# Performance work log

Hardware: AMD Instinct MI355X
Metric: run time of the kernel (lower is better)

The kernel has to match this reference:

```python
import jax, jax.numpy as jnp
import numpy as np

IOU_THRESHOLD = 0.5
CLASS_CONF_THRESHOLD = 0.01
MAX_OUTPUT = 100  # tf.image.non_max_suppression max_output_size


def _nms_indices(boxes, scores, max_out, iou_thr):
    """Fixed-size greedy NMS: returns (idxs[max_out], valid[max_out])."""
    x1, y1, x2, y2 = boxes[:, 0], boxes[:, 1], boxes[:, 2], boxes[:, 3]
    areas = (x2 - x1) * (y2 - y1)

    def body(sc, _):
        i = jnp.argmax(sc)
        valid = sc[i] > 0.0  # score_threshold = 0.0 in tf call
        xx1 = jnp.maximum(x1[i], x1)
        yy1 = jnp.maximum(y1[i], y1)
        xx2 = jnp.minimum(x2[i], x2)
        yy2 = jnp.minimum(y2[i], y2)
        inter = jnp.maximum(xx2 - xx1, 0.0) * jnp.maximum(yy2 - yy1, 0.0)
        union = areas[i] + areas - inter
        iou = jnp.where(union > 0.0, inter / union, 0.0)
        # suppress overlapping boxes (self included, iou=1) only if pick valid
        sc_new = jnp.where((iou > iou_thr) & valid, -1.0, sc)
        return sc_new, (i, valid)

    _, (idxs, valids) = jax.lax.scan(body, scores, None, length=max_out)
    return idxs, valids


def _decode(x, anchors):
    B, H, W, A, C = x.shape  # B == 1
    gw = jnp.float32(W)
    # grid offsets: (col, row) per cell, matching cell_x / transposed cell_y
    cx = jnp.broadcast_to(jnp.arange(W, dtype=jnp.float32).reshape(1, 1, W, 1, 1), (1, H, W, 1, 1))
    cy = jnp.broadcast_to(jnp.arange(H, dtype=jnp.float32).reshape(1, H, 1, 1, 1), (1, H, W, 1, 1))
    grid = jnp.concatenate([cx, cy], axis=-1)  # (1,H,W,1,2)

    xy = (jax.nn.sigmoid(x[..., 0:2]) + grid) / gw                      # (B,H,W,A,2)
    wh = jnp.exp(x[..., 2:4]) * anchors.reshape(1, 1, 1, A, 2) / gw     # (B,H,W,A,2)
    boxes = jnp.concatenate([xy - wh / 2.0, xy + wh / 2.0], axis=-1)    # (B,H,W,A,4)

    conf = jax.nn.sigmoid(x[..., 4:5])                                  # (B,H,W,A,1)
    cls_prob = jax.nn.softmax(x[..., 5:], axis=-1)                      # (B,H,W,A,C-5)
    class_confidence = conf * cls_prob
    masked = jnp.where(class_confidence > CLASS_CONF_THRESHOLD, class_confidence, 0.0)
    classes = jnp.argmax(masked, axis=-1).astype(jnp.int32)             # (B,H,W,A)
    confm = jnp.max(masked, axis=-1)                                    # (B,H,W,A)

    N = H * W * A
    return boxes.reshape(N, 4), confm.reshape(N), classes.reshape(N)


def reference(x, anchors):
    boxes, scores, classes = _decode(x, anchors)
    idxs, valids = _nms_indices(jax.lax.stop_gradient(boxes),
                                jax.lax.stop_gradient(scores),
                                MAX_OUTPUT, IOU_THRESHOLD)
    sel_conf = jnp.where(valids, scores[idxs], 0.0)
    sel_boxes = jnp.where(valids[:, None], boxes[idxs], 0.0)
    sel_classes = jnp.where(valids, classes[idxs], -1)
    return sel_conf, sel_boxes, sel_classes


def setup_inputs() -> dict:
    key = jax.random.key(0)
    k1, k2 = jax.random.split(key)
    x = jax.random.normal(k1, (1, 256, 256, 5, 85), dtype=jnp.float32)
    # anchor priors in grid units (positive widths/heights)
    anchors = jax.random.uniform(k2, (5, 2), dtype=jnp.float32) * 4.0 + 0.5
    return {"x": x, "anchors": anchors}
```

## Files before the change

kernel.cpp:

```cpp
#include <hip/hip_runtime.h>
#include <hip/hip_bf16.h>

#define NROW 327680
#define NCLS 80
#define K_TARGET 1024u
#define CAP 2048u
#define MAXN 2048
#define MAX_OUT 100
#define NBIN 864
#define BIN0 0x3C23
#define HIST_BLOCKS 80
#define ADJW 32
#define ADJC_ROWS 128

#define WS_SCORES 0
#define WS_PART   1310720
#define WS_CNT    1587200
#define WS_KEYS   1587264
#define WS_SORT   1603648
#define WS_CBOX   1620032
#define WS_ADJ    1652800

typedef float f4v __attribute__((ext_vector_type(4)));
typedef f4v f4u __attribute__((aligned(4)));
typedef unsigned long long ull;

__global__ __launch_bounds__(256, 5) void decode_score(
    const float* __restrict__ x, float* __restrict__ scores) {
  __shared__ float sc[24][256];
  const int t = threadIdx.x;
  const int r = blockIdx.x * 256 + t;
  const float* rp = x + (size_t)r * 85;

  float conf_l = rp[4];

  float cl[56];
  #pragma unroll
  for (int k = 0; k < 14; ++k) {
    f4v t4 = *(const f4u*)(rp + 5 + 4 * k);
    cl[4*k+0] = t4.x; cl[4*k+1] = t4.y; cl[4*k+2] = t4.z; cl[4*k+3] = t4.w;
  }
  #pragma unroll
  for (int k = 14; k < 20; ++k) {
    f4v t4 = *(const f4u*)(rp + 5 + 4 * k);
    sc[4*(k-14)+0][t] = t4.x; sc[4*(k-14)+1][t] = t4.y;
    sc[4*(k-14)+2][t] = t4.z; sc[4*(k-14)+3][t] = t4.w;
  }

  float m = cl[0];
  #pragma unroll
  for (int c = 1; c < 56; ++c) { float l = cl[c]; if (l > m) m = l; }
  #pragma unroll
  for (int c = 56; c < 80; ++c) { float l = sc[c-56][t]; if (l > m) m = l; }

  float s = 0.f;
  #pragma unroll
  for (int c = 0; c < 56; ++c) s += expf(cl[c] - m);
  #pragma unroll
  for (int c = 56; c < 80; ++c) s += expf(sc[c-56][t] - m);

  float conf = 1.f / (1.f + expf(-conf_l));
  float best = conf * (1.f / s);
  scores[r] = (best > 0.01f) ? best : 0.f;
}

__global__ __launch_bounds__(1024) void hist_kernel(
    const float* __restrict__ scores, unsigned* __restrict__ part) {
  __shared__ unsigned h[NBIN];
  const int t = threadIdx.x;
  if (t < NBIN) h[t] = 0;
  __syncthreads();

  float4 s4 = ((const float4*)scores)[blockIdx.x * 1024 + t];
  float sv[4] = {s4.x, s4.y, s4.z, s4.w};
  #pragma unroll
  for (int k = 0; k < 4; ++k) {
    float s = sv[k];
    if (s > 0.f) {
      int idx = (int)(__float_as_uint(s) >> 16) - BIN0;
      if (idx > NBIN - 1) idx = NBIN - 1;
      atomicAdd(&h[idx], 1u);
    }
  }
  __syncthreads();
  if (t < NBIN) part[blockIdx.x * NBIN + t] = h[t];
}

__global__ __launch_bounds__(1024) void thresh_kernel(
    const unsigned* __restrict__ part, unsigned* __restrict__ cnt) {
  __shared__ unsigned bufA[1024], bufB[1024];
  const int t = threadIdx.x;

  unsigned colsum = 0;
  if (t < NBIN) {
    unsigned a0 = 0, a1 = 0, a2 = 0, a3 = 0;
    #pragma unroll
    for (int b = 0; b < HIST_BLOCKS; b += 4) {
      a0 += part[(b + 0) * NBIN + t];
      a1 += part[(b + 1) * NBIN + t];
      a2 += part[(b + 2) * NBIN + t];
      a3 += part[(b + 3) * NBIN + t];
    }
    colsum = a0 + a1 + a2 + a3;
  }
  bufA[t] = colsum;
  __syncthreads();

  unsigned* src = bufA; unsigned* dst = bufB;
  for (int d = 1; d < 1024; d <<= 1) {
    unsigned val = src[t] + ((t + d < 1024) ? src[t + d] : 0u);
    dst[t] = val;
    __syncthreads();
    unsigned* tmp = src; src = dst; dst = tmp;
  }
  if (src[t] >= K_TARGET && (t == 1023 || src[t + 1] < K_TARGET)) {
    unsigned T = (unsigned)t;
    if (src[t] > CAP) T += 1;
    cnt[1] = T;
  }
  if (t == 0) {
    if (src[0] < K_TARGET) cnt[1] = 0;
    cnt[0] = 0;
  }
}

__global__ __launch_bounds__(256) void compact_kernel(
    const float* __restrict__ scores, unsigned* __restrict__ cnt,
    ull* __restrict__ keys) {
  __shared__ unsigned blocal, bbase;
  const int t = threadIdx.x;
  if (t == 0) blocal = 0;
  __syncthreads();

  const unsigned T = cnt[1];
  const int gi = blockIdx.x * 256 + t;
  float4 s4 = ((const float4*)scores)[gi];
  float sv[4] = {s4.x, s4.y, s4.z, s4.w};
  ull lk[4]; int nl = 0;
  #pragma unroll
  for (int k = 0; k < 4; ++k) {
    float s = sv[k];
    if (s <= 0.f) continue;
    unsigned bits = __float_as_uint(s);
    int idx = (int)(bits >> 16) - BIN0;
    if (idx > NBIN - 1) idx = NBIN - 1;
    if ((unsigned)idx < T) continue;
    unsigned r = (unsigned)(gi * 4 + k);
    lk[nl++] = ((ull)bits << 32) | (ull)(0xFFFFFFFFu - r);
  }
  unsigned lpos = nl ? atomicAdd(&blocal, (unsigned)nl) : 0u;
  __syncthreads();
  if (t == 0 && blocal) bbase = atomicAdd(&cnt[0], blocal);
  __syncthreads();
  if (nl) {
    unsigned base = bbase + lpos;
    for (int i = 0; i < nl; ++i)
      if (base + i < CAP) keys[base + i] = lk[i];
  }
}

__global__ __launch_bounds__(64) void rank_kernel(
    const float* __restrict__ x, const float* __restrict__ anchors,
    const unsigned* __restrict__ cnt, const ull* __restrict__ keys,
    ull* __restrict__ sorted, float4* __restrict__ cboxg) {
  __shared__ ull lk[MAXN];
  unsigned n = cnt[0]; if (n > CAP) n = CAP;
  const int t = threadIdx.x;
  for (unsigned i = t; i < n; i += 64) lk[i] = keys[i];
  __syncthreads();

  const unsigned i = blockIdx.x * 64 + t;
  if (i >= n) return;
  const ull ki = lk[i];
  unsigned rank = 0;
  #pragma unroll 4
  for (unsigned j = 0; j < n; ++j) rank += (lk[j] > ki) ? 1u : 0u;

  sorted[rank] = ki;

  unsigned r = 0xFFFFFFFFu - (unsigned)(ki & 0xFFFFFFFFull);
  const float* rp = x + (size_t)r * 85;
  float tx = rp[0], ty = rp[1], tw = rp[2], th = rp[3];
  const int a  = (int)(r % 5u);
  const int hw = (int)(r / 5u);
  const float wf = (float)(hw & 255);
  const float hf = (float)(hw >> 8);
  float sx = 1.f / (1.f + expf(-tx));
  float sy = 1.f / (1.f + expf(-ty));
  float xc = (sx + wf) / 256.f;
  float yc = (sy + hf) / 256.f;
  float bw = expf(tw) * anchors[2*a]     / 256.f;
  float bh = expf(th) * anchors[2*a + 1] / 256.f;
  float hwd = bw / 2.f, hhd = bh / 2.f;
  cboxg[rank] = make_float4(xc - hwd, yc - hhd, xc + hwd, yc + hhd);
}

__global__ __launch_bounds__(256) void adj_kernel(
    const unsigned* __restrict__ cnt, const float4* __restrict__ cboxg,
    ull* __restrict__ adj) {
  unsigned n = cnt[0]; if (n > CAP) n = CAP;
  const unsigned i = blockIdx.x;
  if (i >= n) return;
  const float4 bi = cboxg[i];
  const float areai = (bi.z - bi.x) * (bi.w - bi.y);
  const int t = threadIdx.x, wid = t >> 6, lane = t & 63;

  #pragma unroll
  for (int pass = 0; pass < 8; ++pass) {
    unsigned j = (unsigned)(pass * 256 + t);
    bool sup = false;
    if (j < n) {
      float4 bj = cboxg[j];
      float xx1 = fmaxf(bi.x, bj.x), yy1 = fmaxf(bi.y, bj.y);
      float xx2 = fminf(bi.z, bj.z), yy2 = fminf(bi.w, bj.w);
      float inter = fmaxf(xx2 - xx1, 0.f) * fmaxf(yy2 - yy1, 0.f);
      float areaj = (bj.z - bj.x) * (bj.w - bj.y);
      float uni = areai + areaj - inter;
      float iou = (uni > 0.f) ? (inter / uni) : 0.f;
      sup = iou > 0.5f;
    }
    ull m = __ballot(sup);
    if (lane == 0) adj[(size_t)i * ADJW + pass * 4 + wid] = m;
  }
}

__global__ __launch_bounds__(1024) void final_kernel(
    const float* __restrict__ x, const unsigned* __restrict__ cnt,
    const ull* __restrict__ sorted, const float4* __restrict__ cboxg,
    const ull* __restrict__ adjg, float* __restrict__ out) {
  __shared__ ull sk[MAXN];
  __shared__ ull adjc[ADJC_ROWS * ADJW];
  __shared__ int keptcc[MAX_OUT];
  __shared__ int kcls[MAX_OUT];
  __shared__ int knum;
  const int t = threadIdx.x;
  if (t == 0) knum = 0;

  unsigned n = cnt[0]; if (n > CAP) n = CAP;
  for (unsigned i = t; i < n; i += 1024) sk[i] = sorted[i];
  const unsigned ncache = (n < ADJC_ROWS ? n : ADJC_ROWS) * ADJW;
  for (unsigned i = t; i < ncache; i += 1024) adjc[i] = adjg[i];
  __syncthreads();

  if (t < 64) {
    const int lane = t;
    ull mask = 0ull;
    int nk = 0;
    ull rA = 0ull, rB = 0ull;
    if (lane < ADJW) {
      if (n > 0) rA = adjc[0 * ADJW + lane];
      if (n > 1) rB = (1 < ADJC_ROWS) ? adjc[1 * ADJW + lane]
                                      : adjg[1 * ADJW + lane];
    }
    for (unsigned cc = 0; cc < n; ++cc) {
      ull rC = 0ull;
      unsigned pcc = cc + 2;
      if (lane < ADJW && pcc < n)
        rC = (pcc < ADJC_ROWS) ? adjc[pcc * ADJW + lane]
                               : adjg[(size_t)pcc * ADJW + lane];
      const int w = (int)(cc >> 6);
      ull mw = (ull)__shfl((long long)mask, w, 64);
      bool sup = (mw >> (cc & 63u)) & 1ull;
      if (!sup) {
        mask |= rA;
        if (lane == 0) keptcc[nk] = (int)cc;
        ++nk;
        if (nk == MAX_OUT) break;
      }
      rA = rB; rB = rC;
    }
    if (lane == 0) knum = nk;
  }
  __syncthreads();
  const int kn = knum;

  {
    const int wv = t >> 6, lane = t & 63;
    for (int kidx = wv; kidx < kn; kidx += 16) {
      ull key = sk[keptcc[kidx]];
      unsigned r = 0xFFFFFFFFu - (unsigned)(key & 0xFFFFFFFFull);
      const float* rp = x + (size_t)r * 85;
      float l0 = rp[5 + lane];
      unsigned b0 = __float_as_uint(l0);
      b0 = (b0 & 0x80000000u) ? ~b0 : (b0 | 0x80000000u);
      ull kv = ((ull)b0 << 32) | (ull)(0xFFFFFFFFu - lane);
      if (lane < 16) {
        float l1 = rp[5 + 64 + lane];
        unsigned b1 = __float_as_uint(l1);
        b1 = (b1 & 0x80000000u) ? ~b1 : (b1 | 0x80000000u);
        ull kv1 = ((ull)b1 << 32) | (ull)(0xFFFFFFFFu - (64 + lane));
        if (kv1 > kv) kv = kv1;
      }
      #pragma unroll
      for (int d = 32; d >= 1; d >>= 1) {
        ull o = (ull)__shfl_xor((long long)kv, d, 64);
        if (o > kv) kv = o;
      }
      if (lane == 0)
        kcls[kidx] = (int)(0xFFFFFFFFu - (unsigned)(kv & 0xFFFFFFFFull));
    }
  }
  __syncthreads();

  if (t < MAX_OUT) {
    float conf = 0.f; float4 bb = make_float4(0.f, 0.f, 0.f, 0.f); float cf = -1.f;
    if (t < kn) {
      int cc = keptcc[t];
      ull key = sk[cc];
      conf = __uint_as_float((unsigned)(key >> 32));
      bb = cboxg[cc];
      cf = (float)kcls[t];
    }
    out[t] = conf;
    ((float4*)(out + 100))[t] = bb;
    out[500 + t] = cf;
  }
}

extern "C" void kernel_launch(void* const* d_in, const int* in_sizes, int n_in,
                              void* d_out, int out_size, void* d_ws, size_t ws_size,
                              hipStream_t stream) {
  const float* x       = (const float*)d_in[0];
  const float* anchors = (const float*)d_in[1];
  float* out = (float*)d_out;
  char* ws = (char*)d_ws;

  float*    scores = (float*)(ws + WS_SCORES);
  unsigned* part   = (unsigned*)(ws + WS_PART);
  unsigned* cnt    = (unsigned*)(ws + WS_CNT);
  ull*      keys   = (ull*)(ws + WS_KEYS);
  ull*      sorted = (ull*)(ws + WS_SORT);
  float4*   cboxg  = (float4*)(ws + WS_CBOX);
  ull*      adj    = (ull*)(ws + WS_ADJ);

  hipLaunchKernelGGL(decode_score, dim3(NROW / 256), dim3(256),
                     0, stream, x, scores);
  hipLaunchKernelGGL(hist_kernel, dim3(HIST_BLOCKS), dim3(1024),
                     0, stream, scores, part);
  hipLaunchKernelGGL(thresh_kernel, dim3(1), dim3(1024), 0, stream, part, cnt);
  hipLaunchKernelGGL(compact_kernel, dim3(NROW / 1024), dim3(256),
                     0, stream, scores, cnt, keys);
  hipLaunchKernelGGL(rank_kernel, dim3(MAXN / 64), dim3(64),
                     0, stream, x, anchors, cnt, keys, sorted, cboxg);
  hipLaunchKernelGGL(adj_kernel, dim3(MAXN), dim3(256),
                     0, stream, cnt, cboxg, adj);
  hipLaunchKernelGGL(final_kernel, dim3(1), dim3(1024), 0, stream,
                     x, cnt, sorted, cboxg, adj, out);
}
```

Baseline: 236.3 us.

## Fuse NMS pipeline into single cooperative persistent kernel with grid syncs

Replaces the seven separate kernel launches with one cooperative kernel of 512 blocks that moves between stages using grid.sync. The histogram is fused into decode, column sums are parallelized with atomics, and the class argmax is spread across 100 blocks. The aim is to remove launch gaps and the serial single-block stages, in exchange for grid barrier costs and lower occupancy during decode (launch bounds 256,2 with 80 class values held in registers). The original multi-kernel path is kept as a fallback if the cooperative launch fails.

New measurement: 613.6 us. +159.6%, slower.

```diff
diff --git a/kernel.cpp b/kernel.cpp
--- a/kernel.cpp
+++ b/kernel.cpp
@@ -1,5 +1,8 @@
 #include <hip/hip_runtime.h>
 #include <hip/hip_bf16.h>
+#include <hip/hip_cooperative_groups.h>
+
+namespace cg = cooperative_groups;
 
 #define NROW 327680
 #define NCLS 80
@@ -12,18 +15,312 @@
 #define HIST_BLOCKS 80
 #define ADJW 32
 #define ADJC_ROWS 128
+#define MGRID 512
 
 #define WS_SCORES 0
 #define WS_PART   1310720
-#define WS_CNT    1587200
-#define WS_KEYS   1587264
-#define WS_SORT   1603648
-#define WS_CBOX   1620032
-#define WS_ADJ    1652800
+#define WS_COLSUM 3080192
+#define WS_CNT    3084288
+#define WS_KEPT   3084352
+#define WS_KEYS   3084864
+#define WS_SORT   3101248
+#define WS_CBOX   3117632
+#define WS_ADJ    3150400
 
 typedef float f4v __attribute__((ext_vector_type(4)));
 typedef f4v f4u __attribute__((aligned(4)));
 typedef unsigned long long ull;
+
+__global__ __launch_bounds__(256, 2) void mega_kernel(
+    const float* __restrict__ x, const float* __restrict__ anchors,
+    float* __restrict__ out,
+    float* __restrict__ scores, unsigned* __restrict__ part,
+    unsigned* __restrict__ colsum, unsigned* __restrict__ cnt,
+    int* __restrict__ keptg, ull* __restrict__ keys,
+    ull* __restrict__ sorted, float4* __restrict__ cboxg,
+    ull* __restrict__ adj) {
+  cg::grid_group grid = cg::this_grid();
+
+  union SMem {
+    unsigned h[NBIN];
+    struct { unsigned A[1024]; unsigned Bb[1024]; } scan;
+    ull lk[MAXN];
+    struct {
+      ull sk[MAXN];
+      ull adjc[ADJC_ROWS * ADJW];
+      int keptcc[MAX_OUT];
+    } fin;
+  };
+  __shared__ SMem sm;
+  __shared__ unsigned blocal, bbase;
+  __shared__ int knum_s;
+
+  const int t = threadIdx.x;
+  const int B = blockIdx.x;
+
+  for (int i = t; i < NBIN; i += 256) sm.h[i] = 0;
+  if (B == 0) {
+    for (int i = t; i < NBIN; i += 256) colsum[i] = 0;
+    if (t < 16) cnt[t] = 0;
+  }
+  __syncthreads();
+
+  for (int chunk = B; chunk < NROW / 256; chunk += MGRID) {
+    const int r = chunk * 256 + t;
+    const float* rp = x + (size_t)r * 85;
+
+    float conf_l = rp[4];
+    float cl[80];
+    #pragma unroll
+    for (int c = 0; c < 20; ++c) {
+      f4v t4 = *(const f4u*)(rp + 5 + 4 * c);
+      cl[4*c+0] = t4.x; cl[4*c+1] = t4.y; cl[4*c+2] = t4.z; cl[4*c+3] = t4.w;
+    }
+    float m = cl[0];
+    #pragma unroll
+    for (int c = 1; c < NCLS; ++c) { float l = cl[c]; if (l > m) m = l; }
+    float s = 0.f;
+    #pragma unroll
+    for (int c = 0; c < NCLS; ++c) s += expf(cl[c] - m);
+    float conf = 1.f / (1.f + expf(-conf_l));
+    float best = conf * (1.f / s);
+    float sval = (best > 0.01f) ? best : 0.f;
+    scores[r] = sval;
+
+    if (sval > 0.f) {
+      int idx = (int)(__float_as_uint(sval) >> 16) - BIN0;
+      if (idx > NBIN - 1) idx = NBIN - 1;
+      atomicAdd(&sm.h[idx], 1u);
+    }
+  }
+  __syncthreads();
+  for (int b = t; b < NBIN; b += 256) part[(size_t)B * NBIN + b] = sm.h[b];
+  grid.sync();
+
+  {
+    const int u = B * 256 + t;
+    if (u < NBIN * 8) {
+      const int b = u >> 3, seg = u & 7;
+      unsigned s0 = 0, s1 = 0, s2 = 0, s3 = 0;
+      #pragma unroll
+      for (int g = seg * 64; g < seg * 64 + 64; g += 4) {
+        s0 += part[(size_t)(g + 0) * NBIN + b];
+        s1 += part[(size_t)(g + 1) * NBIN + b];
+        s2 += part[(size_t)(g + 2) * NBIN + b];
+        s3 += part[(size_t)(g + 3) * NBIN + b];
+      }
+      atomicAdd(&colsum[b], s0 + s1 + s2 + s3);
+    }
+  }
+  grid.sync();
+
+  if (B == 0) {
+    #pragma unroll
+    for (int e = 0; e < 4; ++e) {
+      int i = t + 256 * e;
+      sm.scan.A[i] = (i < NBIN) ? colsum[i] : 0u;
+    }
+    __syncthreads();
+    unsigned* src = sm.scan.A; unsigned* dst = sm.scan.Bb;
+    for (int d = 1; d < 1024; d <<= 1) {
+      #pragma unroll
+      for (int e = 0; e < 4; ++e) {
+        int i = t + 256 * e;
+        dst[i] = src[i] + ((i + d < 1024) ? src[i + d] : 0u);
+      }
+      __syncthreads();
+      unsigned* tmp = src; src = dst; dst = tmp;
+    }
+    #pragma unroll
+    for (int e = 0; e < 4; ++e) {
+      int i = t + 256 * e;
+      if (src[i] >= K_TARGET && (i == 1023 || src[i + 1] < K_TARGET)) {
+        unsigned T = (unsigned)i;
+        if (src[i] > CAP) T += 1;
+        cnt[1] = T;
+      }
+    }
+    if (t == 0) {
+      if (src[0] < K_TARGET) cnt[1] = 0;
+      cnt[0] = 0;
+    }
+  }
+  grid.sync();
+
+  {
+    const unsigned Tthr = cnt[1];
+    for (int chunk = B; chunk < NROW / 1024; chunk += MGRID) {
+      if (t == 0) blocal = 0;
+      __syncthreads();
+      const int gi = chunk * 256 + t;
+      float4 s4 = ((const float4*)scores)[gi];
+      float sv[4] = {s4.x, s4.y, s4.z, s4.w};
+      ull lkk[4]; int nl = 0;
+      #pragma unroll
+      for (int k = 0; k < 4; ++k) {
+        float s = sv[k];
+        if (s <= 0.f) continue;
+        unsigned bits = __float_as_uint(s);
+        int idx = (int)(bits >> 16) - BIN0;
+        if (idx > NBIN - 1) idx = NBIN - 1;
+        if ((unsigned)idx < Tthr) continue;
+        unsigned r = (unsigned)(gi * 4 + k);
+        lkk[nl++] = ((ull)bits << 32) | (ull)(0xFFFFFFFFu - r);
+      }
+      unsigned lpos = nl ? atomicAdd(&blocal, (unsigned)nl) : 0u;
+      __syncthreads();
+      if (t == 0 && blocal) bbase = atomicAdd(&cnt[0], blocal);
+      __syncthreads();
+      if (nl) {
+        unsigned base = bbase + lpos;
+        for (int i = 0; i < nl; ++i)
+          if (base + i < CAP) keys[base + i] = lkk[i];
+      }
+      __syncthreads();
+    }
+  }
+  grid.sync();
+
+  unsigned n = cnt[0]; if (n > CAP) n = CAP;
+
+  if (B < 8) {
+    for (unsigned i = t; i < n; i += 256) sm.lk[i] = keys[i];
+    __syncthreads();
+    const unsigned i = (unsigned)(B * 256 + t);
+    if (i < n) {
+      const ull ki = sm.lk[i];
+      unsigned rank = 0;
+      #pragma unroll 4
+      for (unsigned j = 0; j < n; ++j) rank += (sm.lk[j] > ki) ? 1u : 0u;
+
+      sorted[rank] = ki;
+
+      unsigned r = 0xFFFFFFFFu - (unsigned)(ki & 0xFFFFFFFFull);
+      const float* rp = x + (size_t)r * 85;
+      float tx = rp[0], ty = rp[1], tw = rp[2], th = rp[3];
+      const int a  = (int)(r % 5u);
+      const int hw = (int)(r / 5u);
+      const float wf = (float)(hw & 255);
+      const float hf = (float)(hw >> 8);
+      float sx = 1.f / (1.f + expf(-tx));
+      float sy = 1.f / (1.f + expf(-ty));
+      float xc = (sx + wf) / 256.f;
+      float yc = (sy + hf) / 256.f;
+      float bw = expf(tw) * anchors[2*a]     / 256.f;
+      float bh = expf(th) * anchors[2*a + 1] / 256.f;
+      float hwd = bw / 2.f, hhd = bh / 2.f;
+      cboxg[rank] = make_float4(xc - hwd, yc - hhd, xc + hwd, yc + hhd);
+    }
+  }
+  grid.sync();
+
+  for (unsigned i = B; i < n; i += MGRID) {
+    const float4 bi = cboxg[i];
+    const float areai = (bi.z - bi.x) * (bi.w - bi.y);
+    const int wid = t >> 6, lane = t & 63;
+    #pragma unroll
+    for (int pass = 0; pass < 8; ++pass) {
+      unsigned j = (unsigned)(pass * 256 + t);
+      bool sup = false;
+      if (j < n) {
+        float4 bj = cboxg[j];
+        float xx1 = fmaxf(bi.x, bj.x), yy1 = fmaxf(bi.y, bj.y);
+        float xx2 = fminf(bi.z, bj.z), yy2 = fminf(bi.w, bj.w);
+        float inter = fmaxf(xx2 - xx1, 0.f) * fmaxf(yy2 - yy1, 0.f);
+        float areaj = (bj.z - bj.x) * (bj.w - bj.y);
+        float uni = areai + areaj - inter;
+        float iou = (uni > 0.f) ? (inter / uni) : 0.f;
+        sup = iou > 0.5f;
+      }
+      ull m = __ballot(sup);
+      if (lane == 0) adj[(size_t)i * ADJW + pass * 4 + wid] = m;
+    }
+  }
+  grid.sync();
+
+  if (B == 0) {
+    for (unsigned i = t; i < n; i += 256) sm.fin.sk[i] = sorted[i];
+    const unsigned ncache = (n < ADJC_ROWS ? n : ADJC_ROWS) * ADJW;
+    for (unsigned i = t; i < ncache; i += 256) sm.fin.adjc[i] = adj[i];
+    if (t == 0) knum_s = 0;
+    __syncthreads();
+
+    if (t < 64) {
+      const int lane = t;
+      ull mask = 0ull;
+      int nk = 0;
+      ull rA = 0ull, rB = 0ull;
+      if (lane < ADJW) {
+        if (n > 0) rA = sm.fin.adjc[0 * ADJW + lane];
+        if (n > 1) rB = (1 < ADJC_ROWS) ? sm.fin.adjc[1 * ADJW + lane]
+                                        : adj[1 * ADJW + lane];
+      }
+      for (unsigned cc = 0; cc < n; ++cc) {
+        ull rC = 0ull;
+        unsigned pcc = cc + 2;
+        if (lane < ADJW && pcc < n)
+          rC = (pcc < ADJC_ROWS) ? sm.fin.adjc[pcc * ADJW + lane]
+                                 : adj[(size_t)pcc * ADJW + lane];
+        const int w = (int)(cc >> 6);
+        ull mw = (ull)__shfl((long long)mask, w, 64);
+        bool sup = (mw >> (cc & 63u)) & 1ull;
+        if (!sup) {
+          mask |= rA;
+          if (lane == 0) sm.fin.keptcc[nk] = (int)cc;
+          ++nk;
+          if (nk == MAX_OUT) break;
+        }
+        rA = rB; rB = rC;
+      }
+      if (lane == 0) knum_s = nk;
+    }
+    __syncthreads();
+    if (t == 0) keptg[0] = knum_s;
+    if (t < MAX_OUT) keptg[1 + t] = (t < knum_s) ? sm.fin.keptcc[t] : -1;
+  }
+  grid.sync();
+
+  if (B < MAX_OUT) {
+    const int kn = keptg[0];
+    const int cc = (B < kn) ? keptg[1 + B] : -1;
+    if (cc >= 0) {
+      const ull key = sorted[cc];
+      const unsigned r = 0xFFFFFFFFu - (unsigned)(key & 0xFFFFFFFFull);
+      if (t < 64) {
+        const int lane = t;
+        const float* rp = x + (size_t)r * 85;
+        float l0 = rp[5 + lane];
+        unsigned b0 = __float_as_uint(l0);
+        b0 = (b0 & 0x80000000u) ? ~b0 : (b0 | 0x80000000u);
+        ull kv = ((ull)b0 << 32) | (ull)(0xFFFFFFFFu - lane);
+        if (lane < 16) {
+          float l1 = rp[5 + 64 + lane];
+          unsigned b1 = __float_as_uint(l1);
+          b1 = (b1 & 0x80000000u) ? ~b1 : (b1 | 0x80000000u);
+          ull kv1 = ((ull)b1 << 32) | (ull)(0xFFFFFFFFu - (64 + lane));
+          if (kv1 > kv) kv = kv1;
+        }
+        #pragma unroll
+        for (int d = 32; d >= 1; d >>= 1) {
+          ull o = (ull)__shfl_xor((long long)kv, d, 64);
+          if (o > kv) kv = o;
+        }
+        if (lane == 0)
+          out[500 + B] = (float)(int)(0xFFFFFFFFu - (unsigned)(kv & 0xFFFFFFFFull));
+      }
+      if (t == 0) {
+        out[B] = __uint_as_float((unsigned)(key >> 32));
+        ((float4*)(out + 100))[B] = cboxg[cc];
+      }
+    } else {
+      if (t == 0) {
+        out[B] = 0.f;
+        ((float4*)(out + 100))[B] = make_float4(0.f, 0.f, 0.f, 0.f);
+        out[500 + B] = -1.f;
+      }
+    }
+  }
+}
 
 __global__ __launch_bounds__(256, 5) void decode_score(
     const float* __restrict__ x, float* __restrict__ scores) {
@@ -33,7 +330,6 @@
   const float* rp = x + (size_t)r * 85;
 
   float conf_l = rp[4];
-
   float cl[56];
   #pragma unroll
   for (int k = 0; k < 14; ++k) {
@@ -46,19 +342,16 @@
     sc[4*(k-14)+0][t] = t4.x; sc[4*(k-14)+1][t] = t4.y;
     sc[4*(k-14)+2][t] = t4.z; sc[4*(k-14)+3][t] = t4.w;
   }
-
   float m = cl[0];
   #pragma unroll
   for (int c = 1; c < 56; ++c) { float l = cl[c]; if (l > m) m = l; }
   #pragma unroll
   for (int c = 56; c < 80; ++c) { float l = sc[c-56][t]; if (l > m) m = l; }
-
   float s = 0.f;
   #pragma unroll
   for (int c = 0; c < 56; ++c) s += expf(cl[c] - m);
   #pragma unroll
   for (int c = 56; c < 80; ++c) s += expf(sc[c-56][t] - m);
-
   float conf = 1.f / (1.f + expf(-conf_l));
   float best = conf * (1.f / s);
   scores[r] = (best > 0.01f) ? best : 0.f;
@@ -70,7 +363,6 @@
   const int t = threadIdx.x;
   if (t < NBIN) h[t] = 0;
   __syncthreads();
-
   float4 s4 = ((const float4*)scores)[blockIdx.x * 1024 + t];
   float sv[4] = {s4.x, s4.y, s4.z, s4.w};
   #pragma unroll
@@ -90,7 +382,6 @@
     const unsigned* __restrict__ part, unsigned* __restrict__ cnt) {
   __shared__ unsigned bufA[1024], bufB[1024];
   const int t = threadIdx.x;
-
   unsigned colsum = 0;
   if (t < NBIN) {
     unsigned a0 = 0, a1 = 0, a2 = 0, a3 = 0;
@@ -105,7 +396,6 @@
   }
   bufA[t] = colsum;
   __syncthreads();
-
   unsigned* src = bufA; unsigned* dst = bufB;
   for (int d = 1; d < 1024; d <<= 1) {
     unsigned val = src[t] + ((t + d < 1024) ? src[t + d] : 0u);
@@ -131,7 +421,6 @@
   const int t = threadIdx.x;
   if (t == 0) blocal = 0;
   __syncthreads();
-
   const unsigned T = cnt[1];
   const int gi = blockIdx.x * 256 + t;
   float4 s4 = ((const float4*)scores)[gi];
@@ -168,16 +457,13 @@
   const int t = threadIdx.x;
   for (unsigned i = t; i < n; i += 64) lk[i] = keys[i];
   __syncthreads();
-
   const unsigned i = blockIdx.x * 64 + t;
   if (i >= n) return;
   const ull ki = lk[i];
   unsigned rank = 0;
   #pragma unroll 4
   for (unsigned j = 0; j < n; ++j) rank += (lk[j] > ki) ? 1u : 0u;
-
   sorted[rank] = ki;
-
   unsigned r = 0xFFFFFFFFu - (unsigned)(ki & 0xFFFFFFFFull);
   const float* rp = x + (size_t)r * 85;
   float tx = rp[0], ty = rp[1], tw = rp[2], th = rp[3];
@@ -204,7 +490,6 @@
   const float4 bi = cboxg[i];
   const float areai = (bi.z - bi.x) * (bi.w - bi.y);
   const int t = threadIdx.x, wid = t >> 6, lane = t & 63;
-
   #pragma unroll
   for (int pass = 0; pass < 8; ++pass) {
     unsigned j = (unsigned)(pass * 256 + t);
@@ -235,13 +520,11 @@
   __shared__ int knum;
   const int t = threadIdx.x;
   if (t == 0) knum = 0;
-
   unsigned n = cnt[0]; if (n > CAP) n = CAP;
   for (unsigned i = t; i < n; i += 1024) sk[i] = sorted[i];
   const unsigned ncache = (n < ADJC_ROWS ? n : ADJC_ROWS) * ADJW;
   for (unsigned i = t; i < ncache; i += 1024) adjc[i] = adjg[i];
   __syncthreads();
-
   if (t < 64) {
     const int lane = t;
     ull mask = 0ull;
@@ -273,7 +556,6 @@
   }
   __syncthreads();
   const int kn = knum;
-
   {
     const int wv = t >> 6, lane = t & 63;
     for (int kidx = wv; kidx < kn; kidx += 16) {
@@ -301,7 +583,6 @@
     }
   }
   __syncthreads();
-
   if (t < MAX_OUT) {
     float conf = 0.f; float4 bb = make_float4(0.f, 0.f, 0.f, 0.f); float cf = -1.f;
     if (t < kn) {
@@ -327,23 +608,35 @@
 
   float*    scores = (float*)(ws + WS_SCORES);
   unsigned* part   = (unsigned*)(ws + WS_PART);
+  unsigned* colsum = (unsigned*)(ws + WS_COLSUM);
   unsigned* cnt    = (unsigned*)(ws + WS_CNT);
+  int*      keptg  = (int*)(ws + WS_KEPT);
   ull*      keys   = (ull*)(ws + WS_KEYS);
   ull*      sorted = (ull*)(ws + WS_SORT);
   float4*   cboxg  = (float4*)(ws + WS_CBOX);
   ull*      adj    = (ull*)(ws + WS_ADJ);
 
-  hipLaunchKernelGGL(decode_score, dim3(NROW / 256), dim3(256),
-                     0, stream, x, scores);
-  hipLaunchKernelGGL(hist_kernel, dim3(HIST_BLOCKS), dim3(1024),
-                     0, stream, scores, part);
-  hipLaunchKernelGGL(thresh_kernel, dim3(1), dim3(1024), 0, stream, part, cnt);
-  hipLaunchKernelGGL(compact_kernel, dim3(NROW / 1024), dim3(256),
-                     0, stream, scores, cnt, keys);
-  hipLaunchKernelGGL(rank_kernel, dim3(MAXN / 64), dim3(64),
-                     0, stream, x, anchors, cnt, keys, sorted, cboxg);
-  hipLaunchKernelGGL(adj_kernel, dim3(MAXN), dim3(256),
-                     0, stream, cnt, cboxg, adj);
-  hipLaunchKernelGGL(final_kernel, dim3(1), dim3(1024), 0, stream,
-                     x, cnt, sorted, cboxg, adj, out);
-}
+  void* args[] = {
+    (void*)&x, (void*)&anchors, (void*)&out,
+    (void*)&scores, (void*)&part, (void*)&colsum, (void*)&cnt,
+    (void*)&keptg, (void*)&keys, (void*)&sorted, (void*)&cboxg, (void*)&adj
+  };
+  hipError_t e = hipLaunchCooperativeKernel(mega_kernel, dim3(MGRID), dim3(256),
+                                            args, 0, stream);
+  if (e != hipSuccess) {
+    (void)hipGetLastError();
+    hipLaunchKernelGGL(decode_score, dim3(NROW / 256), dim3(256),
+                       0, stream, x, scores);
+    hipLaunchKernelGGL(hist_kernel, dim3(HIST_BLOCKS), dim3(1024),
+                       0, stream, scores, part);
+    hipLaunchKernelGGL(thresh_kernel, dim3(1), dim3(1024), 0, stream, part, cnt);
+    hipLaunchKernelGGL(compact_kernel, dim3(NROW / 1024), dim3(256),
+                       0, stream, scores, cnt, keys);
+    hipLaunchKernelGGL(rank_kernel, dim3(MAXN / 64), dim3(64),
+                       0, stream, x, anchors, cnt, keys, sorted, cboxg);
+    hipLaunchKernelGGL(adj_kernel, dim3(MAXN), dim3(256),
+                       0, stream, cnt, cboxg, adj);
+    hipLaunchKernelGGL(final_kernel, dim3(1), dim3(1024), 0, stream,
+                       x, cnt, sorted, cboxg, adj, out);
+  }
+}
```
